# Kernel tuning notes

Hardware: AMD Instinct MI355X
Metric: run time of the kernel (lower is better)

The kernel has to match this reference:

```python
import jax, jax.numpy as jnp
import numpy as np

B, T, D = 2, 4096, 512
H, K = 8, 64
F = 2048
EPS = 1e-5


def _layer_norm(x, scale, offset):
    mean = jnp.mean(x, axis=-1, keepdims=True)
    var = jnp.var(x, axis=-1, keepdims=True)
    inv = scale * jax.lax.rsqrt(var + EPS)
    return (x - mean) * inv + offset


def setup_inputs() -> dict:
    key = jax.random.key(0)
    ks = jax.random.split(key, 12)
    s = lambda fan_in: (2.0 / fan_in) ** 0.5  # VarianceScaling(2.0) std
    inputs = jax.random.normal(ks[0], (B, T, D), jnp.float32)
    return {
        "inputs": inputs,
        "ln1_scale": jnp.ones((D,), jnp.float32),
        "ln1_offset": jnp.zeros((D,), jnp.float32),
        "wq": jax.random.normal(ks[1], (D, H * K), jnp.float32) * s(D),
        "bq": jnp.zeros((H * K,), jnp.float32),
        "wk": jax.random.normal(ks[2], (D, H * K), jnp.float32) * s(D),
        "bk": jnp.zeros((H * K,), jnp.float32),
        "wv": jax.random.normal(ks[3], (D, H * K), jnp.float32) * s(D),
        "bv": jnp.zeros((H * K,), jnp.float32),
        "wo": jax.random.normal(ks[4], (H * K, D), jnp.float32) * s(H * K),
        "bo": jnp.zeros((D,), jnp.float32),
        "ln2_scale": jnp.ones((D,), jnp.float32),
        "ln2_offset": jnp.zeros((D,), jnp.float32),
        "w1": jax.random.normal(ks[5], (D, F), jnp.float32) * (1.0 / D) ** 0.5,
        "b1": jnp.zeros((F,), jnp.float32),
        "w2": jax.random.normal(ks[6], (F, D), jnp.float32) * (1.0 / F) ** 0.5,
        "b2": jnp.zeros((D,), jnp.float32),
    }


def reference(inputs, ln1_scale, ln1_offset, wq, bq, wk, bk, wv, bv, wo, bo,
              ln2_scale, ln2_offset, w1, b1, w2, b2):
    # --- pre-attention LayerNorm ---
    x1 = _layer_norm(inputs, ln1_scale, ln1_offset)
    # --- multi-head attention (eval mode, no mask) ---
    q = (x1 @ wq + bq).reshape(B, T, H, K)
    k = (x1 @ wk + bk).reshape(B, T, H, K)
    v = (x1 @ wv + bv).reshape(B, T, H, K)
    logits = jnp.einsum('bthd,bshd->bhts', q, k) / jnp.sqrt(jnp.asarray(K, q.dtype))
    attn = jax.nn.softmax(logits, axis=-1)
    ctx = jnp.einsum('bhts,bshd->bthd', attn, v).reshape(B, T, H * K)
    attn_out = ctx @ wo + bo
    # --- residual ---
    x = inputs + attn_out
    # --- pre-FFN LayerNorm + GELU FFN ---
    y = _layer_norm(x, ln2_scale, ln2_offset)
    ff = jax.nn.gelu(y @ w1 + b1) @ w2 + b2
    return x + ff
```

## Files before the change

kernel.cpp:

```cpp
#include <hip/hip_runtime.h>
#include <hip/hip_bf16.h>

typedef __attribute__((ext_vector_type(4))) float f32x4;
typedef __attribute__((ext_vector_type(8))) short short8;

#define DEV __device__ __forceinline__

DEV short f2bf(float f) {
    union { float f; unsigned u; } a; a.f = f;
    unsigned r = a.u + 0x7fffu + ((a.u >> 16) & 1u);
    return (short)(r >> 16);
}

DEV float bf2f(short s) {
    union { unsigned u; float f; } a;
    a.u = ((unsigned)(unsigned short)s) << 16;
    return a.f;
}

DEV unsigned cvt_pk_bf16(float a, float b) {
    unsigned r;
    asm("v_cvt_pk_bf16_f32 %0, %1, %2" : "=v"(r) : "v"(a), "v"(b));
    return r;
}

DEV float exp2_fast(float x) { return __builtin_amdgcn_exp2f(x); }

DEV float gelu_f(float x) {
    float u = 0.7978845608028654f * (x + 0.044715f * x * x * x);
    float e = __expf(2.0f * u);
    float t = 1.0f - 2.0f / (e + 1.0f);
    return 0.5f * x * (1.0f + t);
}

__global__ __launch_bounds__(256) void ln_kernel(const float* __restrict__ x,
                                                 const float* __restrict__ scale,
                                                 const float* __restrict__ offset,
                                                 short* __restrict__ out) {
    const int wid = threadIdx.x >> 6, lane = threadIdx.x & 63;
    const long row = (long)blockIdx.x * 4 + wid;
    const float* xr = x + row * 512;
    f32x4 v0 = *(const f32x4*)&xr[lane * 8];
    f32x4 v1 = *(const f32x4*)&xr[lane * 8 + 4];
    float s = 0.f, sq = 0.f;
#pragma unroll
    for (int i = 0; i < 4; i++) {
        s += v0[i] + v1[i];
        sq += v0[i] * v0[i] + v1[i] * v1[i];
    }
#pragma unroll
    for (int m = 1; m < 64; m <<= 1) { s += __shfl_xor(s, m); sq += __shfl_xor(sq, m); }
    float mean = s * (1.0f / 512.0f);
    float var = sq * (1.0f / 512.0f) - mean * mean;
    float inv = rsqrtf(var + 1e-5f);
    f32x4 sc0 = *(const f32x4*)&scale[lane * 8];
    f32x4 sc1 = *(const f32x4*)&scale[lane * 8 + 4];
    f32x4 of0 = *(const f32x4*)&offset[lane * 8];
    f32x4 of1 = *(const f32x4*)&offset[lane * 8 + 4];
    short8 o;
#pragma unroll
    for (int i = 0; i < 4; i++) {
        o[i]     = f2bf((v0[i] - mean) * inv * sc0[i] + of0[i]);
        o[4 + i] = f2bf((v1[i] - mean) * inv * sc1[i] + of1[i]);
    }
    *(short8*)&out[row * 512 + lane * 8] = o;
}

__global__ __launch_bounds__(256) void prep_kernel(const float* __restrict__ wq,
                                                   const float* __restrict__ wk,
                                                   const float* __restrict__ wv,
                                                   const float* __restrict__ wo,
                                                   const float* __restrict__ w1,
                                                   const float* __restrict__ w2,
                                                   const float* __restrict__ bq,
                                                   const float* __restrict__ bk,
                                                   const float* __restrict__ bv,
                                                   short* __restrict__ wqkvt,
                                                   short* __restrict__ wot,
                                                   short* __restrict__ w1t,
                                                   short* __restrict__ w2t,
                                                   float* __restrict__ bqkv) {
    const int bid = blockIdx.x;
    if (bid == 768) {
        for (int i = threadIdx.x; i < 512; i += 256) {
            bqkv[i] = bq[i]; bqkv[512 + i] = bk[i]; bqkv[1024 + i] = bv[i];
        }
        return;
    }
    const float* src; short* dst; int Kd, N, kt, nt;
    if (bid < 256) {
        Kd = 512; N = 512;
        const int which = bid >> 6, local = bid & 63;
        kt = local & 7; nt = local >> 3;
        if (which == 0)      { src = wq; dst = wqkvt; }
        else if (which == 1) { src = wk; dst = wqkvt + 512 * 512; }
        else if (which == 2) { src = wv; dst = wqkvt + 2 * 512 * 512; }
        else                 { src = wo; dst = wot; }
    } else if (bid < 512) {
        src = w1; dst = w1t; Kd = 512; N = 2048;
        const int local = bid - 256; kt = local & 7; nt = local >> 3;
    } else {
        src = w2; dst = w2t; Kd = 2048; N = 512;
        const int local = bid - 512; kt = local & 31; nt = local >> 5;
    }
    __shared__ float tile[64][65];
    const int k0 = kt * 64, n0 = nt * 64;
    const int tid = threadIdx.x;
#pragma unroll
    for (int ld = 0; ld < 4; ld++) {
        int li = ld * 1024 + tid * 4;
        int r = li >> 6, c = li & 63;
        f32x4 tv = *(const f32x4*)&src[(long)(k0 + r) * N + n0 + c];
        tile[r][c] = tv[0]; tile[r][c + 1] = tv[1];
        tile[r][c + 2] = tv[2]; tile[r][c + 3] = tv[3];
    }
    __syncthreads();
#pragma unroll
    for (int st = 0; st < 2; st++) {
        int li = st * 2048 + tid * 8;
        int r = li >> 6, c = li & 63;
        short8 o;
#pragma unroll
        for (int i = 0; i < 8; i++) o[i] = f2bf(tile[c + i][r]);
        *(short8*)&dst[(long)(n0 + r) * Kd + k0 + c] = o;
    }
}

template <bool GELU_ACT, bool OUT_BF16, bool RESID>
__global__ __launch_bounds__(256) void gemm_bt(const short* __restrict__ A,
                                               const short* __restrict__ Bt,
                                               const float* __restrict__ bias,
                                               const float* __restrict__ resid,
                                               void* __restrict__ Cout,
                                               int M, int N, int Kd) {
    __shared__ short Asm[128][72];
    __shared__ short Bsm[128][72];
    const int tid = threadIdx.x;
    const int wid = tid >> 6, lane = tid & 63;
    const int lr = lane & 15, lg = lane >> 4;
    const int row0 = blockIdx.x * 128, col0 = blockIdx.y * 128;
    const int wm = (wid >> 1) * 64, wn = (wid & 1) * 64;

    f32x4 acc[4][4];
#pragma unroll
    for (int m = 0; m < 4; m++)
#pragma unroll
        for (int n = 0; n < 4; n++)
#pragma unroll
            for (int j = 0; j < 4; j++) acc[m][n][j] = 0.f;

    for (int k0 = 0; k0 < Kd; k0 += 64) {
#pragma unroll
        for (int ld = 0; ld < 4; ld++) {
            int li = ld * 2048 + tid * 8;
            int r = li >> 6, c = li & 63;
            *(short8*)&Asm[r][c] = *(const short8*)&A[(long)(row0 + r) * Kd + k0 + c];
            *(short8*)&Bsm[r][c] = *(const short8*)&Bt[(long)(col0 + r) * Kd + k0 + c];
        }
        __syncthreads();
#pragma unroll
        for (int kk = 0; kk < 64; kk += 32) {
            short8 af[4], bf[4];
#pragma unroll
            for (int m = 0; m < 4; m++) af[m] = *(const short8*)&Asm[wm + m * 16 + lr][kk + lg * 8];
#pragma unroll
            for (int n = 0; n < 4; n++) bf[n] = *(const short8*)&Bsm[wn + n * 16 + lr][kk + lg * 8];
#pragma unroll
            for (int m = 0; m < 4; m++)
#pragma unroll
                for (int n = 0; n < 4; n++)
                    acc[m][n] = __builtin_amdgcn_mfma_f32_16x16x32_bf16(af[m], bf[n], acc[m][n], 0, 0, 0);
        }
        __syncthreads();
    }

#pragma unroll
    for (int m = 0; m < 4; m++) {
#pragma unroll
        for (int n = 0; n < 4; n++) {
#pragma unroll
            for (int j = 0; j < 4; j++) {
                int r = row0 + wm + m * 16 + lg * 4 + j;
                int c = col0 + wn + n * 16 + lr;
                float v = acc[m][n][j] + bias[c];
                if constexpr (GELU_ACT) v = gelu_f(v);
                if constexpr (RESID) v += resid[(long)r * N + c];
                if constexpr (OUT_BF16) ((short*)Cout)[(long)r * N + c] = f2bf(v);
                else                    ((float*)Cout)[(long)r * N + c] = v;
            }
        }
    }
}

__global__ __launch_bounds__(256) void attn_kernel(const short* __restrict__ q,
                                                   const short* __restrict__ k,
                                                   const short* __restrict__ v,
                                                   short* __restrict__ ctx) {
    __shared__ short Ksm[128][72];
    __shared__ short Vsm[64][136];
    __shared__ short Psm[4][16][136];
    const int tid = threadIdx.x, wid = tid >> 6, lane = tid & 63;
    const int lr = lane & 15, lg = lane >> 4;
    const int bh = blockIdx.y, b = bh >> 3, h = bh & 7;
    const int t0 = blockIdx.x * 128;
    const long base = (long)b * 4096 * 1536 + h * 64;

    short8 qf[2][2];
#pragma unroll
    for (int rg = 0; rg < 2; rg++) {
        const long qoff = base + (long)(t0 + wid * 32 + rg * 16 + lr) * 1536 + lg * 8;
        short8 q0 = *(const short8*)&q[qoff];
        short8 q1 = *(const short8*)&q[qoff + 32];
#pragma unroll
        for (int i = 0; i < 8; i++) {
            qf[rg][0][i] = f2bf(bf2f(q0[i]) * 0.18033688f);
            qf[rg][1][i] = f2bf(bf2f(q1[i]) * 0.18033688f);
        }
    }

    f32x4 o[2][4];
    float mrow[8], lrow[8];
#pragma unroll
    for (int rg = 0; rg < 2; rg++)
#pragma unroll
        for (int n = 0; n < 4; n++)
#pragma unroll
            for (int j = 0; j < 4; j++) o[rg][n][j] = 0.f;
#pragma unroll
    for (int j = 0; j < 8; j++) { mrow[j] = -1e30f; lrow[j] = 0.f; }

    const int skey = tid >> 3, sd = (tid & 7) * 8, sm = tid & 7;
    short8 kreg[4], vreg[4];
#pragma unroll
    for (int p = 0; p < 4; p++) {
        long off = base + (long)(p * 32 + skey) * 1536 + sd;
        kreg[p] = *(const short8*)&k[off];
        vreg[p] = *(const short8*)&v[off];
    }

    for (int s0 = 0; s0 < 4096; s0 += 128) {
        __syncthreads();
#pragma unroll
        for (int p = 0; p < 4; p++) {
            int key = p * 32 + skey;
            *(short8*)&Ksm[key][sd] = kreg[p];
            int kc = key ^ (sm << 3);
#pragma unroll
            for (int i = 0; i < 8; i++) Vsm[sd + i][kc] = vreg[p][i];
        }
        __syncthreads();
        if (s0 + 128 < 4096) {
#pragma unroll
            for (int p = 0; p < 4; p++) {
                long off = base + (long)(s0 + 128 + p * 32 + skey) * 1536 + sd;
                kreg[p] = *(const short8*)&k[off];
                vreg[p] = *(const short8*)&v[off];
            }
        }

#pragma unroll
        for (int rg = 0; rg < 2; rg++) {
            f32x4 s[8];
#pragma unroll
            for (int c = 0; c < 8; c++) { s[c][0] = 0.f; s[c][1] = 0.f; s[c][2] = 0.f; s[c][3] = 0.f; }
            __builtin_amdgcn_s_setprio(1);
#pragma unroll
            for (int c = 0; c < 8; c++) {
                short8 kf0 = *(const short8*)&Ksm[c * 16 + lr][lg * 8];
                short8 kf1 = *(const short8*)&Ksm[c * 16 + lr][32 + lg * 8];
                s[c] = __builtin_amdgcn_mfma_f32_16x16x32_bf16(qf[rg][0], kf0, s[c], 0, 0, 0);
                s[c] = __builtin_amdgcn_mfma_f32_16x16x32_bf16(qf[rg][1], kf1, s[c], 0, 0, 0);
            }
            __builtin_amdgcn_s_setprio(0);

#pragma unroll
            for (int j = 0; j < 4; j++) {
                const int r8 = rg * 4 + j;
                float m01 = fmaxf(s[0][j], s[1][j]), m23 = fmaxf(s[2][j], s[3][j]);
                float m45 = fmaxf(s[4][j], s[5][j]), m67 = fmaxf(s[6][j], s[7][j]);
                float mx = fmaxf(fmaxf(m01, m23), fmaxf(m45, m67));
                mx = fmaxf(mx, __shfl_xor(mx, 1));
                mx = fmaxf(mx, __shfl_xor(mx, 2));
                mx = fmaxf(mx, __shfl_xor(mx, 4));
                mx = fmaxf(mx, __shfl_xor(mx, 8));
                float mn = mrow[r8];
                if (!__all(mx <= mn + 8.0f)) {
                    mn = fmaxf(mrow[r8], mx);
                    float alpha = exp2_fast(mrow[r8] - mn);
                    mrow[r8] = mn;
                    lrow[r8] *= alpha;
#pragma unroll
                    for (int n = 0; n < 4; n++) o[rg][n][j] *= alpha;
                }
                float rs = 0.f;
#pragma unroll
                for (int c = 0; c < 8; c++) {
                    float e = exp2_fast(s[c][j] - mn);
                    s[c][j] = e;
                    rs += e;
                }
                rs += __shfl_xor(rs, 1);
                rs += __shfl_xor(rs, 2);
                rs += __shfl_xor(rs, 4);
                rs += __shfl_xor(rs, 8);
                lrow[r8] += rs;
            }

#pragma unroll
            for (int j = 0; j < 4; j++) {
                short* prow = &Psm[wid][lg * 4 + j][lr];
#pragma unroll
                for (int c = 0; c < 8; c += 2) {
                    unsigned pk = cvt_pk_bf16(s[c][j], s[c + 1][j]);
                    prow[c * 16]      = (short)(pk & 0xffff);
                    prow[c * 16 + 16] = (short)(pk >> 16);
                }
            }
            short8 pa[4];
#pragma unroll
            for (int kk = 0; kk < 4; kk++) pa[kk] = *(const short8*)&Psm[wid][lr][kk * 32 + lg * 8];

            __builtin_amdgcn_s_setprio(1);
#pragma unroll
            for (int n = 0; n < 4; n++) {
                const int vrow = n * 16 + lr;
                const int vsw = ((vrow >> 3) & 7) << 3;
#pragma unroll
                for (int kk = 0; kk < 4; kk++) {
                    short8 vf = *(const short8*)&Vsm[vrow][(kk * 32 + lg * 8) ^ vsw];
                    o[rg][n] = __builtin_amdgcn_mfma_f32_16x16x32_bf16(pa[kk], vf, o[rg][n], 0, 0, 0);
                }
            }
            __builtin_amdgcn_s_setprio(0);
        }
    }

    const long cb = (long)b * 4096 * 512 + h * 64 + (long)(t0 + wid * 32) * 512;
#pragma unroll
    for (int rg = 0; rg < 2; rg++)
#pragma unroll
        for (int j = 0; j < 4; j++) {
            float il = 1.0f / lrow[rg * 4 + j];
#pragma unroll
            for (int n = 0; n < 4; n++)
                ctx[cb + (long)(rg * 16 + lg * 4 + j) * 512 + n * 16 + lr] = f2bf(o[rg][n][j] * il);
        }
}

extern "C" void kernel_launch(void* const* d_in, const int* in_sizes, int n_in,
                              void* d_out, int out_size, void* d_ws, size_t ws_size,
                              hipStream_t stream) {
    (void)in_sizes; (void)n_in; (void)out_size; (void)ws_size;
    const float* inputs = (const float*)d_in[0];
    const float* ln1_s  = (const float*)d_in[1];
    const float* ln1_o  = (const float*)d_in[2];
    const float* wq     = (const float*)d_in[3];
    const float* bq     = (const float*)d_in[4];
    const float* wk     = (const float*)d_in[5];
    const float* bk     = (const float*)d_in[6];
    const float* wv     = (const float*)d_in[7];
    const float* bv     = (const float*)d_in[8];
    const float* wo     = (const float*)d_in[9];
    const float* bo     = (const float*)d_in[10];
    const float* ln2_s  = (const float*)d_in[11];
    const float* ln2_o  = (const float*)d_in[12];
    const float* w1     = (const float*)d_in[13];
    const float* b1     = (const float*)d_in[14];
    const float* w2     = (const float*)d_in[15];
    const float* b2     = (const float*)d_in[16];
    float* out = (float*)d_out;

    char* p = (char*)d_ws;
    auto alloc = [&](size_t bytes) { void* r = (void*)p; p += (bytes + 255) & ~(size_t)255; return r; };
    short* x1    = (short*)alloc((size_t)8192 * 512 * 2);
    short* qkvb  = (short*)alloc((size_t)8192 * 1536 * 2);
    short* ctxb  = (short*)alloc((size_t)8192 * 512 * 2);
    short* yb    = (short*)alloc((size_t)8192 * 512 * 2);
    short* hb    = (short*)alloc((size_t)8192 * 2048 * 2);
    short* wqkvt = (short*)alloc((size_t)1536 * 512 * 2);
    short* wot   = (short*)alloc((size_t)512 * 512 * 2);
    short* w1t   = (short*)alloc((size_t)2048 * 512 * 2);
    short* w2t   = (short*)alloc((size_t)512 * 2048 * 2);
    float* bqkv  = (float*)alloc((size_t)1536 * 4);

    dim3 blk(256);
    prep_kernel<<<769, blk, 0, stream>>>(wq, wk, wv, wo, w1, w2, bq, bk, bv,
                                         wqkvt, wot, w1t, w2t, bqkv);
    ln_kernel<<<2048, blk, 0, stream>>>(inputs, ln1_s, ln1_o, x1);
    gemm_bt<false, true, false><<<dim3(64, 12), blk, 0, stream>>>(x1, wqkvt, bqkv, nullptr, qkvb, 8192, 1536, 512);
    attn_kernel<<<dim3(32, 16), blk, 0, stream>>>(qkvb, qkvb + 512, qkvb + 1024, ctxb);
    gemm_bt<false, false, true><<<dim3(64, 4), blk, 0, stream>>>(ctxb, wot, bo, inputs, out, 8192, 512, 512);
    ln_kernel<<<2048, blk, 0, stream>>>(out, ln2_s, ln2_o, yb);
    gemm_bt<true, true, false><<<dim3(64, 16), blk, 0, stream>>>(yb, w1t, b1, nullptr, hb, 8192, 2048, 512);
    gemm_bt<false, false, true><<<dim3(64, 4), blk, 0, stream>>>(hb, w2t, b2, out, out, 8192, 512, 2048);
}
```

Measured before the change: 416.0 us.

## Split attention over key halves with merge kernel; swizzled LDS and direct global-to-LDS loads

```diff
diff --git a/kernel.cpp b/kernel.cpp
--- a/kernel.cpp
+++ b/kernel.cpp
@@ -25,6 +25,12 @@
 }
 
 DEV float exp2_fast(float x) { return __builtin_amdgcn_exp2f(x); }
+
+DEV void gload16(const short* g, short* l) {
+    __builtin_amdgcn_global_load_lds(
+        (__attribute__((address_space(1))) void*)g,
+        (__attribute__((address_space(3))) void*)l, 16, 0, 0);
+}
 
 DEV float gelu_f(float x) {
     float u = 0.7978845608028654f * (x + 0.044715f * x * x * x);
@@ -133,8 +139,8 @@
                                                const float* __restrict__ resid,
                                                void* __restrict__ Cout,
                                                int M, int N, int Kd) {
-    __shared__ short Asm[128][72];
-    __shared__ short Bsm[128][72];
+    __shared__ short Asm[128][64];
+    __shared__ short Bsm[128][64];
     const int tid = threadIdx.x;
     const int wid = tid >> 6, lane = tid & 63;
     const int lr = lane & 15, lg = lane >> 4;
@@ -149,22 +155,25 @@
 #pragma unroll
             for (int j = 0; j < 4; j++) acc[m][n][j] = 0.f;
 
+    const int swr = (lr & 7) << 3;
+
     for (int k0 = 0; k0 < Kd; k0 += 64) {
 #pragma unroll
         for (int ld = 0; ld < 4; ld++) {
-            int li = ld * 2048 + tid * 8;
-            int r = li >> 6, c = li & 63;
-            *(short8*)&Asm[r][c] = *(const short8*)&A[(long)(row0 + r) * Kd + k0 + c];
-            *(short8*)&Bsm[r][c] = *(const short8*)&Bt[(long)(col0 + r) * Kd + k0 + c];
+            int off = ld * 2048 + tid * 8;
+            int r = off >> 6, c = off & 63;
+            int sc = c ^ ((r & 7) << 3);
+            gload16(&A[(long)(row0 + r) * Kd + k0 + sc], &Asm[0][0] + off);
+            gload16(&Bt[(long)(col0 + r) * Kd + k0 + sc], &Bsm[0][0] + off);
         }
         __syncthreads();
 #pragma unroll
         for (int kk = 0; kk < 64; kk += 32) {
             short8 af[4], bf[4];
 #pragma unroll
-            for (int m = 0; m < 4; m++) af[m] = *(const short8*)&Asm[wm + m * 16 + lr][kk + lg * 8];
-#pragma unroll
-            for (int n = 0; n < 4; n++) bf[n] = *(const short8*)&Bsm[wn + n * 16 + lr][kk + lg * 8];
+            for (int m = 0; m < 4; m++) af[m] = *(const short8*)&Asm[wm + m * 16 + lr][(kk + lg * 8) ^ swr];
+#pragma unroll
+            for (int n = 0; n < 4; n++) bf[n] = *(const short8*)&Bsm[wn + n * 16 + lr][(kk + lg * 8) ^ swr];
 #pragma unroll
             for (int m = 0; m < 4; m++)
 #pragma unroll
@@ -195,14 +204,18 @@
 __global__ __launch_bounds__(256) void attn_kernel(const short* __restrict__ q,
                                                    const short* __restrict__ k,
                                                    const short* __restrict__ v,
-                                                   short* __restrict__ ctx) {
-    __shared__ short Ksm[128][72];
+                                                   float* __restrict__ opart,
+                                                   float* __restrict__ mpart,
+                                                   float* __restrict__ lpart) {
+    __shared__ short Ksm[128][64];
     __shared__ short Vsm[64][136];
     __shared__ short Psm[4][16][136];
     const int tid = threadIdx.x, wid = tid >> 6, lane = tid & 63;
     const int lr = lane & 15, lg = lane >> 4;
     const int bh = blockIdx.y, b = bh >> 3, h = bh & 7;
     const int t0 = blockIdx.x * 128;
+    const int split = blockIdx.z;
+    const int s_begin = split * 2048, s_end = s_begin + 2048;
     const long base = (long)b * 4096 * 1536 + h * 64;
 
     short8 qf[2][2];
@@ -233,23 +246,23 @@
     short8 kreg[4], vreg[4];
 #pragma unroll
     for (int p = 0; p < 4; p++) {
-        long off = base + (long)(p * 32 + skey) * 1536 + sd;
+        long off = base + (long)(s_begin + p * 32 + skey) * 1536 + sd;
         kreg[p] = *(const short8*)&k[off];
         vreg[p] = *(const short8*)&v[off];
     }
 
-    for (int s0 = 0; s0 < 4096; s0 += 128) {
+    for (int s0 = s_begin; s0 < s_end; s0 += 128) {
         __syncthreads();
 #pragma unroll
         for (int p = 0; p < 4; p++) {
             int key = p * 32 + skey;
-            *(short8*)&Ksm[key][sd] = kreg[p];
+            *(short8*)&Ksm[key][sd ^ ((key & 7) << 3)] = kreg[p];
             int kc = key ^ (sm << 3);
 #pragma unroll
             for (int i = 0; i < 8; i++) Vsm[sd + i][kc] = vreg[p][i];
         }
         __syncthreads();
-        if (s0 + 128 < 4096) {
+        if (s0 + 128 < s_end) {
 #pragma unroll
             for (int p = 0; p < 4; p++) {
                 long off = base + (long)(s0 + 128 + p * 32 + skey) * 1536 + sd;
@@ -258,26 +271,32 @@
             }
         }
 
+        f32x4 s[2][8];
+#pragma unroll
+        for (int rg = 0; rg < 2; rg++)
+#pragma unroll
+            for (int c = 0; c < 8; c++) { s[rg][c][0] = 0.f; s[rg][c][1] = 0.f; s[rg][c][2] = 0.f; s[rg][c][3] = 0.f; }
+        __builtin_amdgcn_s_setprio(1);
+        const int ksw = (lr & 7) << 3;
+#pragma unroll
+        for (int c = 0; c < 8; c++) {
+            const int krow = c * 16 + lr;
+            short8 kf0 = *(const short8*)&Ksm[krow][(lg * 8) ^ ksw];
+            short8 kf1 = *(const short8*)&Ksm[krow][(32 + lg * 8) ^ ksw];
+            s[0][c] = __builtin_amdgcn_mfma_f32_16x16x32_bf16(qf[0][0], kf0, s[0][c], 0, 0, 0);
+            s[0][c] = __builtin_amdgcn_mfma_f32_16x16x32_bf16(qf[0][1], kf1, s[0][c], 0, 0, 0);
+            s[1][c] = __builtin_amdgcn_mfma_f32_16x16x32_bf16(qf[1][0], kf0, s[1][c], 0, 0, 0);
+            s[1][c] = __builtin_amdgcn_mfma_f32_16x16x32_bf16(qf[1][1], kf1, s[1][c], 0, 0, 0);
+        }
+        __builtin_amdgcn_s_setprio(0);
+
 #pragma unroll
         for (int rg = 0; rg < 2; rg++) {
-            f32x4 s[8];
-#pragma unroll
-            for (int c = 0; c < 8; c++) { s[c][0] = 0.f; s[c][1] = 0.f; s[c][2] = 0.f; s[c][3] = 0.f; }
-            __builtin_amdgcn_s_setprio(1);
-#pragma unroll
-            for (int c = 0; c < 8; c++) {
-                short8 kf0 = *(const short8*)&Ksm[c * 16 + lr][lg * 8];
-                short8 kf1 = *(const short8*)&Ksm[c * 16 + lr][32 + lg * 8];
-                s[c] = __builtin_amdgcn_mfma_f32_16x16x32_bf16(qf[rg][0], kf0, s[c], 0, 0, 0);
-                s[c] = __builtin_amdgcn_mfma_f32_16x16x32_bf16(qf[rg][1], kf1, s[c], 0, 0, 0);
-            }
-            __builtin_amdgcn_s_setprio(0);
-
 #pragma unroll
             for (int j = 0; j < 4; j++) {
                 const int r8 = rg * 4 + j;
-                float m01 = fmaxf(s[0][j], s[1][j]), m23 = fmaxf(s[2][j], s[3][j]);
-                float m45 = fmaxf(s[4][j], s[5][j]), m67 = fmaxf(s[6][j], s[7][j]);
+                float m01 = fmaxf(s[rg][0][j], s[rg][1][j]), m23 = fmaxf(s[rg][2][j], s[rg][3][j]);
+                float m45 = fmaxf(s[rg][4][j], s[rg][5][j]), m67 = fmaxf(s[rg][6][j], s[rg][7][j]);
                 float mx = fmaxf(fmaxf(m01, m23), fmaxf(m45, m67));
                 mx = fmaxf(mx, __shfl_xor(mx, 1));
                 mx = fmaxf(mx, __shfl_xor(mx, 2));
@@ -295,8 +314,8 @@
                 float rs = 0.f;
 #pragma unroll
                 for (int c = 0; c < 8; c++) {
-                    float e = exp2_fast(s[c][j] - mn);
-                    s[c][j] = e;
+                    float e = exp2_fast(s[rg][c][j] - mn);
+                    s[rg][c][j] = e;
                     rs += e;
                 }
                 rs += __shfl_xor(rs, 1);
@@ -311,7 +330,7 @@
                 short* prow = &Psm[wid][lg * 4 + j][lr];
 #pragma unroll
                 for (int c = 0; c < 8; c += 2) {
-                    unsigned pk = cvt_pk_bf16(s[c][j], s[c + 1][j]);
+                    unsigned pk = cvt_pk_bf16(s[rg][c][j], s[rg][c + 1][j]);
                     prow[c * 16]      = (short)(pk & 0xffff);
                     prow[c * 16 + 16] = (short)(pk >> 16);
                 }
@@ -335,16 +354,51 @@
         }
     }
 
-    const long cb = (long)b * 4096 * 512 + h * 64 + (long)(t0 + wid * 32) * 512;
+    const long rowbase = (long)b * 4096 + t0 + wid * 32;
+    const long ob = ((long)split * 8192 + rowbase) * 512 + h * 64;
 #pragma unroll
     for (int rg = 0; rg < 2; rg++)
 #pragma unroll
-        for (int j = 0; j < 4; j++) {
-            float il = 1.0f / lrow[rg * 4 + j];
+        for (int j = 0; j < 4; j++)
 #pragma unroll
             for (int n = 0; n < 4; n++)
-                ctx[cb + (long)(rg * 16 + lg * 4 + j) * 512 + n * 16 + lr] = f2bf(o[rg][n][j] * il);
-        }
+                opart[ob + (long)(rg * 16 + lg * 4 + j) * 512 + n * 16 + lr] = o[rg][n][j];
+    if (lr == 0) {
+#pragma unroll
+        for (int rg = 0; rg < 2; rg++)
+#pragma unroll
+            for (int j = 0; j < 4; j++) {
+                long idx = ((long)split * 8192 + rowbase + rg * 16 + lg * 4 + j) * 8 + h;
+                mpart[idx] = mrow[rg * 4 + j];
+                lpart[idx] = lrow[rg * 4 + j];
+            }
+    }
+}
+
+__global__ __launch_bounds__(256) void attn_merge(const float* __restrict__ op,
+                                                  const float* __restrict__ mp,
+                                                  const float* __restrict__ lp,
+                                                  short* __restrict__ ctx) {
+    const int wid = threadIdx.x >> 6, lane = threadIdx.x & 63;
+    const long row = (long)blockIdx.x * 4 + wid;
+    const int c0 = lane * 8, h = c0 >> 6;
+    float m0 = mp[row * 8 + h], m1 = mp[(8192 + row) * 8 + h];
+    float l0 = lp[row * 8 + h], l1 = lp[(8192 + row) * 8 + h];
+    float M = fmaxf(m0, m1);
+    float w0 = exp2_fast(m0 - M), w1 = exp2_fast(m1 - M);
+    float inv = 1.0f / (w0 * l0 + w1 * l1);
+    w0 *= inv; w1 *= inv;
+    f32x4 a0 = *(const f32x4*)&op[row * 512 + c0];
+    f32x4 a1 = *(const f32x4*)&op[row * 512 + c0 + 4];
+    f32x4 b0 = *(const f32x4*)&op[(8192 + row) * 512 + c0];
+    f32x4 b1 = *(const f32x4*)&op[(8192 + row) * 512 + c0 + 4];
+    short8 o;
+#pragma unroll
+    for (int i = 0; i < 4; i++) {
+        o[i]     = f2bf(w0 * a0[i] + w1 * b0[i]);
+        o[4 + i] = f2bf(w0 * a1[i] + w1 * b1[i]);
+    }
+    *(short8*)&ctx[row * 512 + c0] = o;
 }
 
 extern "C" void kernel_launch(void* const* d_in, const int* in_sizes, int n_in,
@@ -382,13 +436,17 @@
     short* w1t   = (short*)alloc((size_t)2048 * 512 * 2);
     short* w2t   = (short*)alloc((size_t)512 * 2048 * 2);
     float* bqkv  = (float*)alloc((size_t)1536 * 4);
+    float* opart = (float*)alloc((size_t)2 * 8192 * 512 * 4);
+    float* mpart = (float*)alloc((size_t)2 * 8192 * 8 * 4);
+    float* lpart = (float*)alloc((size_t)2 * 8192 * 8 * 4);
 
     dim3 blk(256);
     prep_kernel<<<769, blk, 0, stream>>>(wq, wk, wv, wo, w1, w2, bq, bk, bv,
                                          wqkvt, wot, w1t, w2t, bqkv);
     ln_kernel<<<2048, blk, 0, stream>>>(inputs, ln1_s, ln1_o, x1);
     gemm_bt<false, true, false><<<dim3(64, 12), blk, 0, stream>>>(x1, wqkvt, bqkv, nullptr, qkvb, 8192, 1536, 512);
-    attn_kernel<<<dim3(32, 16), blk, 0, stream>>>(qkvb, qkvb + 512, qkvb + 1024, ctxb);
+    attn_kernel<<<dim3(32, 16, 2), blk, 0, stream>>>(qkvb, qkvb + 512, qkvb + 1024, opart, mpart, lpart);
+    attn_merge<<<2048, blk, 0, stream>>>(opart, mpart, lpart, ctxb);
     gemm_bt<false, false, true><<<dim3(64, 4), blk, 0, stream>>>(ctxb, wot, bo, inputs, out, 8192, 512, 512);
     ln_kernel<<<2048, blk, 0, stream>>>(out, ln2_s, ln2_o, yb);
     gemm_bt<true, true, false><<<dim3(64, 16), blk, 0, stream>>>(yb, w1t, b1, nullptr, hb, 8192, 2048, 512);
```

Result: slower. 505.9 us (+21.6%).
